# Performance work log

Hardware: AMD Instinct MI355X
Metric: run time of the kernel (lower is better)

The kernel has to match this reference:

```python
import jax, jax.numpy as jnp
import numpy as np
import math

H = 12  # num_heads
LOGIT_SCALE_MAX = math.log(1.0 / 0.01)  # ~4.60517


def setup_inputs() -> dict:
    key = jax.random.key(0)
    ks = jax.random.split(key, 4)
    L, N, C = 1024, 8, 768
    scale = (C // H) ** -0.5
    return {
        "x": jax.random.normal(ks[0], (L, N, C), jnp.float32),
        "in_proj_weight": jax.random.normal(ks[1], (3 * C, C), jnp.float32) * scale,
        "in_proj_bias": jnp.zeros((3 * C,), jnp.float32),
        "logit_scale": jnp.full((H, 1, 1), jnp.log(10.0), jnp.float32),
        "head_scale": jnp.ones((H, 1, 1), jnp.float32),
        "out_w": jax.random.normal(ks[2], (C, C), jnp.float32) * scale,
        "out_b": jnp.zeros((C,), jnp.float32),
    }


def _normalize(t, eps=1e-12):
    # torch F.normalize: x / max(||x||, eps)
    n = jnp.linalg.norm(t, axis=-1, keepdims=True)
    return t / jnp.maximum(n, eps)


def reference(x, in_proj_weight, in_proj_bias, logit_scale, head_scale, out_w, out_b):
    L, N, C = x.shape
    D = C // H
    qkv = x @ in_proj_weight.T + in_proj_bias  # (L, N, 3C)
    q, k, v = jnp.split(qkv, 3, axis=-1)

    def to_heads(t):  # (L, N, C) -> (N, H, L, D); matches view(L, N*H, D).transpose(0,1)
        return t.reshape(L, N, H, D).transpose(1, 2, 0, 3)

    q, k, v = to_heads(q), to_heads(k), to_heads(v)
    # scaled-cosine attention: cosine sim * clamped-exp learnable logit scale
    attn = jnp.einsum('nhld,nhmd->nhlm', _normalize(q), _normalize(k))  # (N,H,L,L)
    ls = jnp.exp(jnp.minimum(logit_scale, LOGIT_SCALE_MAX))  # (H,1,1)
    attn = attn * ls[None]
    attn = jax.nn.softmax(attn, axis=-1)
    o = jnp.einsum('nhlm,nhmd->nhld', attn, v)  # (N,H,L,D)
    o = o * head_scale[None]  # per-head scale
    o = o.transpose(2, 0, 1, 3).reshape(L, N, C)  # back to (L, N, C)
    return o @ out_w.T + out_b
```

## Files before the change

kernel.cpp:

```cpp
#include <hip/hip_runtime.h>
#include <stdint.h>
#include <math.h>

typedef unsigned short u16;
typedef _Float16 f16;
typedef __attribute__((ext_vector_type(4))) float f32x4;
typedef __attribute__((ext_vector_type(8))) f16 h8;
typedef __attribute__((ext_vector_type(4))) f16 h4;
typedef __attribute__((ext_vector_type(2))) f16 h2;
typedef __attribute__((ext_vector_type(2))) __fp16 fp16x2;
typedef __attribute__((ext_vector_type(2))) unsigned int u32x2;
typedef __attribute__((ext_vector_type(4))) unsigned int u32x4;
typedef __attribute__((ext_vector_type(4))) unsigned short u16x4;
typedef __attribute__((ext_vector_type(8))) unsigned short u16x8;

typedef const __attribute__((address_space(1))) u16 gas_u16;
typedef __attribute__((address_space(3))) u16 las_u16;

#define MFMA32(a,b,c) __builtin_amdgcn_mfma_f32_16x16x32_f16((a),(b),(c),0,0,0)
#define MFMA16(a,b,c) __builtin_amdgcn_mfma_f32_16x16x16f16((a),(b),(c),0,0,0)

__device__ __forceinline__ float h2f(u16 h){ f16 x; __builtin_memcpy(&x,&h,2); return (float)x; }
__device__ __forceinline__ u16 f2h(float f){ f16 x = (f16)f; u16 u; __builtin_memcpy(&u,&x,2); return u; }

__device__ __forceinline__ float fast_exp2(float x){
#if __has_builtin(__builtin_amdgcn_exp2f)
  return __builtin_amdgcn_exp2f(x);
#else
  return exp2f(x);
#endif
}

__device__ __forceinline__ h2 pkrtz(float a, float b){
  fp16x2 t = __builtin_amdgcn_cvt_pkrtz(a, b);
  h2 r; __builtin_memcpy(&r, &t, 4);
  return r;
}

#define NA4 1572864
#define NB4 442368
#define NC4 147456
__global__ __launch_bounds__(256) void cvt3_kernel(
    const float* __restrict__ a, u16* __restrict__ da,
    const float* __restrict__ b, u16* __restrict__ db,
    const float* __restrict__ c, u16* __restrict__ dc)
{
  int i = blockIdx.x*256 + threadIdx.x;
  const float* s; u16* d; int off;
  if (i < NA4)            { s = a; d = da; off = i; }
  else if (i < NA4+NB4)   { s = b; d = db; off = i - NA4; }
  else if (i < NA4+NB4+NC4){ s = c; d = dc; off = i - NA4 - NB4; }
  else return;
  f32x4 v = ((const f32x4*)s)[off];
  u16x4 o;
  o[0]=f2h(v[0]); o[1]=f2h(v[1]); o[2]=f2h(v[2]); o[3]=f2h(v[3]);
  ((u16x4*)d)[off] = o;
}

__global__ __launch_bounds__(256) void gemm_kernel(
    const u16* __restrict__ A, const u16* __restrict__ B, const float* __restrict__ bias,
    int mode, u16* __restrict__ qh, u16* __restrict__ kh, u16* __restrict__ vtp,
    float* __restrict__ outp, const float* __restrict__ lsb)
{
  __shared__ u16 lA[2][128*64];
  __shared__ u16 lB[2][128*64];
  const int tid = threadIdx.x;
  const int lane = tid & 63;
  const int w = tid >> 6, wr = w >> 1, wc = w & 1;
  const int lo = lane & 15, hi = lane >> 4;

  const int bx = blockIdx.x, by = blockIdx.y;

  f32x4 zero = {0.f,0.f,0.f,0.f};
  f32x4 acc[4][4];
#pragma unroll
  for (int a=0;a<4;a++)
#pragma unroll
    for (int b=0;b<4;b++) acc[a][b] = zero;
  const u16* Ag = A + (size_t)bx*128*768;
  const u16* Bg = B + (size_t)by*128*768;
  const int srow = tid >> 3;
  const int scol = (((tid & 7) ^ (srow & 7)) * 8);

#define STAGE(buf, kt) do { \
    _Pragma("unroll") \
    for (int j=0;j<4;j++) { \
      __builtin_amdgcn_global_load_lds((gas_u16*)(Ag + (size_t)(j*32+srow)*768 + (kt) + scol), (las_u16*)(&lA[buf][j*2048 + tid*8]), 16, 0, 0); \
      __builtin_amdgcn_global_load_lds((gas_u16*)(Bg + (size_t)(j*32+srow)*768 + (kt) + scol), (las_u16*)(&lB[buf][j*2048 + tid*8]), 16, 0, 0); \
    } \
  } while(0)

  STAGE(0, 0);
#pragma unroll
  for (int t = 0; t < 12; ++t) {
    const int cur = t & 1;
    if (t < 11) {
      STAGE(cur^1, (t+1)*64);
      asm volatile("s_waitcnt vmcnt(8)" ::: "memory");
    } else {
      asm volatile("s_waitcnt vmcnt(0)" ::: "memory");
    }
    __builtin_amdgcn_sched_barrier(0);
    __builtin_amdgcn_s_barrier();
#pragma unroll
    for (int kk=0;kk<2;kk++) {
      h8 af[4], bfr[4];
#pragma unroll
      for (int mf=0; mf<4; mf++) {
        int r = wr*64 + mf*16 + lo;
        af[mf]  = *(const h8*)(&lA[cur][r*64 + (((hi + 4*kk) ^ (lo & 7)) * 8)]);
      }
#pragma unroll
      for (int nf=0; nf<4; nf++) {
        int r = wc*64 + nf*16 + lo;
        bfr[nf] = *(const h8*)(&lB[cur][r*64 + (((hi + 4*kk) ^ (lo & 7)) * 8)]);
      }
#pragma unroll
      for (int mf=0; mf<4; mf++)
#pragma unroll
        for (int nf=0; nf<4; nf++)
          acc[mf][nf] = MFMA32(af[mf], bfr[nf], acc[mf][nf]);
    }
    asm volatile("s_waitcnt lgkmcnt(0)" ::: "memory");
    __builtin_amdgcn_sched_barrier(0);
    __builtin_amdgcn_s_barrier();
  }
#undef STAGE

  const int r0 = bx*128 + wr*64;
  const int j0 = by*128 + wc*64;
  if (mode == 0) {
    const int p = (j0 >= 1536) ? 2 : ((j0 >= 768) ? 1 : 0);
    float bi[4];
#pragma unroll
    for (int nf=0;nf<4;nf++) bi[nf] = bias[j0 + nf*16 + lo];
    if (p == 2) {
      u16* Tt = (wc == 0) ? (u16*)lA : (u16*)lB;
      const int cbase = wr*16;
#pragma unroll
      for (int mf=0; mf<4; mf++)
#pragma unroll
        for (int nf=0; nf<4; nf++) {
          int d = nf*16 + lo;
          int c = cbase + mf*4 + hi;
          u16x4 pk;
#pragma unroll
          for (int i=0;i<4;i++) pk[i] = f2h(acc[mf][nf][i] + bi[nf]);
          *(u16x4*)(Tt + d*128 + ((c ^ ((d & 7) << 2)) << 2)) = pk;
        }
      __syncthreads();
      const int hh0 = 2*by - 24;
#pragma unroll
      for (int kq=0; kq<8; kq++) {
        int idx = tid + kq*256;
        int nn  = idx & 7;
        int d   = (idx >> 3) & 63;
        int lh  = (idx >> 9) & 1;
        int wcc = idx >> 10;
        const u16* Ts = (wcc == 0) ? (const u16*)lA : (const u16*)lB;
        u16x8 v8;
#pragma unroll
        for (int ll=0; ll<8; ll++) {
          int rl = (lh*8 + ll)*8 + nn;
          int c  = rl >> 2;
          v8[ll] = Ts[d*128 + ((c ^ ((d & 7) << 2)) << 2) + (rl & 3)];
        }
        size_t off = (((size_t)nn*12 + hh0 + wcc)*64 + d)*1024 + (size_t)bx*16 + lh*8;
        *(u16x8*)(vtp + off) = v8;
      }
    } else {
      const int c0 = j0 - p*768;
      const int hh = c0 >> 6;
      u16* dst = (p==0) ? qh : kh;
      float qsc = 1.0f;
      if (p == 0) qsc = __expf(fminf(lsb[hh], 4.6051701859880913680f)) * 1.4426950408889634f;
#pragma unroll
      for (int mf=0; mf<4; mf++)
#pragma unroll
        for (int i=0;i<4;i++) {
          int r = r0 + mf*16 + 4*hi + i;
          int n = r & 7, l = r >> 3;
          float v[4]; float ss = 0.f;
#pragma unroll
          for (int nf=0;nf<4;nf++){ v[nf] = acc[mf][nf][i] + bi[nf]; ss += v[nf]*v[nf]; }
          ss += __shfl_xor(ss, 1);
          ss += __shfl_xor(ss, 2);
          ss += __shfl_xor(ss, 4);
          ss += __shfl_xor(ss, 8);
          float sc = qsc / fmaxf(sqrtf(ss), 1e-12f);
          size_t base = (((size_t)n*12 + hh)*1024 + l)*64;
#pragma unroll
          for (int nf=0;nf<4;nf++)
            dst[base + nf*16 + lo] = f2h(v[nf]*sc);
        }
    }
  } else {
#pragma unroll
    for (int nf=0; nf<4; nf++) {
      int j = j0 + nf*16 + lo;
      float bi = bias[j];
#pragma unroll
      for (int mf=0; mf<4; mf++)
#pragma unroll
        for (int i=0;i<4;i++) {
          int r = r0 + mf*16 + 4*hi + i;
          outp[(size_t)r*768 + j] = acc[mf][nf][i] + bi;
        }
    }
  }
}

__global__ __launch_bounds__(256, 6) void flash_kernel(
    const u16* __restrict__ qh, const u16* __restrict__ kh, const u16* __restrict__ vt,
    u16* __restrict__ obuf, const float* __restrict__ hsv, const float* __restrict__ lsp)
{
  __shared__ u16 lK[64*64];
  __shared__ u16 lVT[64*64];
  const int lin = blockIdx.y*16 + blockIdx.x;
  const int xcd = lin & 7, g = lin >> 3;
  const int nh = xcd + 8*(g >> 4);
  const int qt = g & 15;
  const int h = nh % 12, n = nh / 12;
  const u16* Qp = qh + (size_t)nh*65536;
  const u16* Kp = kh + (size_t)nh*65536;
  const u16* Vp = vt + (size_t)nh*65536;
  const int tid = threadIdx.x, lane = tid & 63, w = tid >> 6;
  const int lo = lane & 15, hi = lane >> 4;
  const int e = lo & 7;

  h8 qa0, qa1;
  {
    const u16* qrow = Qp + (size_t)(qt*64 + w*16 + lo)*64 + hi*8;
    qa0 = *(const h8*)qrow;
    qa1 = *(const h8*)(qrow + 32);
  }
  const f32x4 zero = {0.f,0.f,0.f,0.f};
  f32x4 oA[4] = {zero,zero,zero,zero};
  f32x4 lA4 = zero;
  const h4 ones = {(f16)1.f,(f16)1.f,(f16)1.f,(f16)1.f};

  float OFF;
  {
    float b = __expf(fminf(lsp[h], 4.6051701859880913680f)) * 1.4426950408889634f;
    OFF = fmaxf(b - 15.5f, 0.f);
  }

  const int sr = tid >> 2;
  const int c4 = tid & 3;
  const int sx1 = sr & 7;
  const int sx2 = (sr & 7) << 1;

  u32x4 ka, kb, va, vb;
  ka = *(const u32x4*)(Kp + (size_t)sr*64 + c4*16);
  kb = *(const u32x4*)(Kp + (size_t)sr*64 + c4*16 + 8);
  va = *(const u32x4*)(Vp + (size_t)sr*1024 + c4*16);
  vb = *(const u32x4*)(Vp + (size_t)sr*1024 + c4*16 + 8);

  for (int t = 0; t < 16; ++t) {
    {
      u16* kr = lK + sr*64;
      *(u32x4*)(kr + (((2*c4)   ^ sx1) << 3)) = ka;
      *(u32x4*)(kr + (((2*c4+1) ^ sx1) << 3)) = kb;
      u16* vr = lVT + sr*64;
      *(u32x2*)(vr + (((( 0|c4) ^ sx2) << 2))) = (u32x2){va[0], va[1]};
      *(u32x2*)(vr + (((( 4|c4) ^ sx2) << 2))) = (u32x2){va[2], va[3]};
      *(u32x2*)(vr + (((( 8|c4) ^ sx2) << 2))) = (u32x2){vb[0], vb[1]};
      *(u32x2*)(vr + ((((12|c4) ^ sx2) << 2))) = (u32x2){vb[2], vb[3]};
    }
    asm volatile("s_waitcnt lgkmcnt(0)" ::: "memory");
    __builtin_amdgcn_sched_barrier(0);
    __builtin_amdgcn_s_barrier();
    if (t < 15) {
      ka = *(const u32x4*)(Kp + (size_t)(t+1)*4096 + (size_t)sr*64 + c4*16);
      kb = *(const u32x4*)(Kp + (size_t)(t+1)*4096 + (size_t)sr*64 + c4*16 + 8);
      va = *(const u32x4*)(Vp + (size_t)sr*1024 + (t+1)*64 + c4*16);
      vb = *(const u32x4*)(Vp + (size_t)sr*1024 + (t+1)*64 + c4*16 + 8);
    }
    f32x4 sa[4];
#pragma unroll
    for (int kf=0; kf<4; kf++) {
      const u16* krow = lK + (kf*16 + lo)*64;
      h8 k0 = *(const h8*)(krow + (((hi  ) ^ e) << 3));
      h8 k1 = *(const h8*)(krow + (((hi+4) ^ e) << 3));
      sa[kf] = MFMA32(k1, qa1, MFMA32(k0, qa0, zero));
    }
    if (OFF != 0.f) {
#pragma unroll
      for (int kf=0;kf<4;kf++)
#pragma unroll
        for (int i=0;i<4;i++) sa[kf][i] -= OFF;
    }
    h4 pa[4];
#pragma unroll
    for (int kf=0;kf<4;kf++) {
      h2 a01 = pkrtz(fast_exp2(sa[kf][0]), fast_exp2(sa[kf][1]));
      h2 a23 = pkrtz(fast_exp2(sa[kf][2]), fast_exp2(sa[kf][3]));
      pa[kf] = __builtin_shufflevector(a01, a23, 0, 1, 2, 3);
    }
#pragma unroll
    for (int kf=0;kf<4;kf++) lA4 = MFMA16(ones, pa[kf], lA4);
#pragma unroll
    for (int db=0; db<4; db++) {
      const u16* vrow = lVT + (db*16 + lo)*64;
      h8 v01 = *(const h8*)(vrow + ((((2*hi  ) ^ e) << 3)));
      h8 v23 = *(const h8*)(vrow + ((((2*hi+1) ^ e) << 3)));
      oA[db] = MFMA16(__builtin_shufflevector(v01, v01, 0,1,2,3), pa[0], oA[db]);
      oA[db] = MFMA16(__builtin_shufflevector(v01, v01, 4,5,6,7), pa[1], oA[db]);
      oA[db] = MFMA16(__builtin_shufflevector(v23, v23, 0,1,2,3), pa[2], oA[db]);
      oA[db] = MFMA16(__builtin_shufflevector(v23, v23, 4,5,6,7), pa[3], oA[db]);
    }
    asm volatile("s_waitcnt lgkmcnt(0)" ::: "memory");
    __builtin_amdgcn_sched_barrier(0);
    __builtin_amdgcn_s_barrier();
  }
  float inv = hsv[h] / lA4[0];
  int l = qt*64 + w*16 + lo;
  u16* dst = obuf + ((size_t)l*8 + n)*768 + h*64;
#pragma unroll
  for (int db=0; db<4; db++) {
    u16x4 pk;
#pragma unroll
    for (int i=0;i<4;i++) pk[i] = f2h(oA[db][i] * inv);
    *(u16x4*)(dst + db*16 + hi*4) = pk;
  }
}

extern "C" void kernel_launch(void* const* d_in, const int* in_sizes, int n_in,
                              void* d_out, int out_size, void* d_ws, size_t ws_size,
                              hipStream_t stream)
{
  (void)in_sizes; (void)n_in; (void)out_size; (void)ws_size;
  const float* x  = (const float*)d_in[0];
  const float* w1 = (const float*)d_in[1];
  const float* b1 = (const float*)d_in[2];
  const float* ls = (const float*)d_in[3];
  const float* hs = (const float*)d_in[4];
  const float* w2 = (const float*)d_in[5];
  const float* b2 = (const float*)d_in[6];
  float* out = (float*)d_out;

  u16* x_bf  = (u16*)d_ws;
  u16* w1_bf = x_bf  + 6291456;
  u16* w2_bf = w1_bf + 1769472;
  u16* qh    = w2_bf + 589824;
  u16* kh    = qh    + 6291456;
  u16* vt    = kh    + 6291456;
  u16* ob    = x_bf;

  cvt3_kernel<<<8448, 256, 0, stream>>>(x, x_bf, w1, w1_bf, w2, w2_bf);
  gemm_kernel<<<dim3(64,18), 256, 0, stream>>>(x_bf, w1_bf, b1, 0, qh, kh, vt, nullptr, ls);
  flash_kernel<<<dim3(16,96), 256, 0, stream>>>(qh, kh, vt, ob, hs, ls);
  gemm_kernel<<<dim3(64,6), 256, 0, stream>>>(ob, w2_bf, b2, 1, nullptr, nullptr, nullptr, out, ls);
}
```

Baseline: 123.7 us.

## Double query rows per flash block to reuse K/V tiles across two fragments

Each flash-attention block now handles 128 query rows instead of 64, with every wave computing two 16-row fragments that share the same K and V loads from LDS. The grid is halved and launch bounds drop to 3 blocks per SM to make room for the extra accumulator registers. The aim is to halve the global-to-LDS traffic per query and cut LDS reads per MFMA. The cost is lower occupancy, fewer blocks (768) in the grid, and higher register pressure.

```diff
diff --git a/kernel.cpp b/kernel.cpp
--- a/kernel.cpp
+++ b/kernel.cpp
@@ -210,16 +210,16 @@
   }
 }
 
-__global__ __launch_bounds__(256, 6) void flash_kernel(
+__global__ __launch_bounds__(256, 3) void flash_kernel(
     const u16* __restrict__ qh, const u16* __restrict__ kh, const u16* __restrict__ vt,
     u16* __restrict__ obuf, const float* __restrict__ hsv, const float* __restrict__ lsp)
 {
   __shared__ u16 lK[64*64];
   __shared__ u16 lVT[64*64];
-  const int lin = blockIdx.y*16 + blockIdx.x;
+  const int lin = blockIdx.y*8 + blockIdx.x;
   const int xcd = lin & 7, g = lin >> 3;
-  const int nh = xcd + 8*(g >> 4);
-  const int qt = g & 15;
+  const int nh = xcd + 8*(g >> 3);
+  const int qt = g & 7;
   const int h = nh % 12, n = nh / 12;
   const u16* Qp = qh + (size_t)nh*65536;
   const u16* Kp = kh + (size_t)nh*65536;
@@ -228,15 +228,16 @@
   const int lo = lane & 15, hi = lane >> 4;
   const int e = lo & 7;
 
-  h8 qa0, qa1;
+  h8 qa0, qa1, qb0, qb1;
   {
-    const u16* qrow = Qp + (size_t)(qt*64 + w*16 + lo)*64 + hi*8;
-    qa0 = *(const h8*)qrow;
-    qa1 = *(const h8*)(qrow + 32);
+    const u16* qrow = Qp + (size_t)(qt*128 + w*32 + lo)*64 + hi*8;
+    qa0 = *(const h8*)qrow;          qa1 = *(const h8*)(qrow + 32);
+    qb0 = *(const h8*)(qrow + 1024); qb1 = *(const h8*)(qrow + 1024 + 32);
   }
   const f32x4 zero = {0.f,0.f,0.f,0.f};
   f32x4 oA[4] = {zero,zero,zero,zero};
-  f32x4 lA4 = zero;
+  f32x4 oB[4] = {zero,zero,zero,zero};
+  f32x4 lA4 = zero, lB4 = zero;
   const h4 ones = {(f16)1.f,(f16)1.f,(f16)1.f,(f16)1.f};
 
   float OFF;
@@ -276,52 +277,71 @@
       va = *(const u32x4*)(Vp + (size_t)sr*1024 + (t+1)*64 + c4*16);
       vb = *(const u32x4*)(Vp + (size_t)sr*1024 + (t+1)*64 + c4*16 + 8);
     }
-    f32x4 sa[4];
+    f32x4 sa[4], sb[4];
 #pragma unroll
     for (int kf=0; kf<4; kf++) {
       const u16* krow = lK + (kf*16 + lo)*64;
       h8 k0 = *(const h8*)(krow + (((hi  ) ^ e) << 3));
       h8 k1 = *(const h8*)(krow + (((hi+4) ^ e) << 3));
       sa[kf] = MFMA32(k1, qa1, MFMA32(k0, qa0, zero));
+      sb[kf] = MFMA32(k1, qb1, MFMA32(k0, qb0, zero));
     }
     if (OFF != 0.f) {
 #pragma unroll
       for (int kf=0;kf<4;kf++)
 #pragma unroll
-        for (int i=0;i<4;i++) sa[kf][i] -= OFF;
-    }
-    h4 pa[4];
+        for (int i=0;i<4;i++) { sa[kf][i] -= OFF; sb[kf][i] -= OFF; }
+    }
+    h4 pa[4], pb[4];
 #pragma unroll
     for (int kf=0;kf<4;kf++) {
       h2 a01 = pkrtz(fast_exp2(sa[kf][0]), fast_exp2(sa[kf][1]));
       h2 a23 = pkrtz(fast_exp2(sa[kf][2]), fast_exp2(sa[kf][3]));
       pa[kf] = __builtin_shufflevector(a01, a23, 0, 1, 2, 3);
-    }
-#pragma unroll
-    for (int kf=0;kf<4;kf++) lA4 = MFMA16(ones, pa[kf], lA4);
+      h2 b01 = pkrtz(fast_exp2(sb[kf][0]), fast_exp2(sb[kf][1]));
+      h2 b23 = pkrtz(fast_exp2(sb[kf][2]), fast_exp2(sb[kf][3]));
+      pb[kf] = __builtin_shufflevector(b01, b23, 0, 1, 2, 3);
+    }
+#pragma unroll
+    for (int kf=0;kf<4;kf++) {
+      lA4 = MFMA16(ones, pa[kf], lA4);
+      lB4 = MFMA16(ones, pb[kf], lB4);
+    }
 #pragma unroll
     for (int db=0; db<4; db++) {
       const u16* vrow = lVT + (db*16 + lo)*64;
       h8 v01 = *(const h8*)(vrow + ((((2*hi  ) ^ e) << 3)));
       h8 v23 = *(const h8*)(vrow + ((((2*hi+1) ^ e) << 3)));
-      oA[db] = MFMA16(__builtin_shufflevector(v01, v01, 0,1,2,3), pa[0], oA[db]);
-      oA[db] = MFMA16(__builtin_shufflevector(v01, v01, 4,5,6,7), pa[1], oA[db]);
-      oA[db] = MFMA16(__builtin_shufflevector(v23, v23, 0,1,2,3), pa[2], oA[db]);
-      oA[db] = MFMA16(__builtin_shufflevector(v23, v23, 4,5,6,7), pa[3], oA[db]);
+      h4 f0 = __builtin_shufflevector(v01, v01, 0,1,2,3);
+      h4 f1 = __builtin_shufflevector(v01, v01, 4,5,6,7);
+      h4 f2 = __builtin_shufflevector(v23, v23, 0,1,2,3);
+      h4 f3 = __builtin_shufflevector(v23, v23, 4,5,6,7);
+      oA[db] = MFMA16(f0, pa[0], oA[db]);
+      oB[db] = MFMA16(f0, pb[0], oB[db]);
+      oA[db] = MFMA16(f1, pa[1], oA[db]);
+      oB[db] = MFMA16(f1, pb[1], oB[db]);
+      oA[db] = MFMA16(f2, pa[2], oA[db]);
+      oB[db] = MFMA16(f2, pb[2], oB[db]);
+      oA[db] = MFMA16(f3, pa[3], oA[db]);
+      oB[db] = MFMA16(f3, pb[3], oB[db]);
     }
     asm volatile("s_waitcnt lgkmcnt(0)" ::: "memory");
     __builtin_amdgcn_sched_barrier(0);
     __builtin_amdgcn_s_barrier();
   }
-  float inv = hsv[h] / lA4[0];
-  int l = qt*64 + w*16 + lo;
-  u16* dst = obuf + ((size_t)l*8 + n)*768 + h*64;
+  float hsc = hsv[h];
+  float invA = hsc / lA4[0];
+  float invB = hsc / lB4[0];
+  int l0 = qt*128 + w*32 + lo;
+  u16* dA = obuf + ((size_t)l0*8 + n)*768 + h*64;
+  u16* dB = obuf + ((size_t)(l0+16)*8 + n)*768 + h*64;
 #pragma unroll
   for (int db=0; db<4; db++) {
-    u16x4 pk;
-#pragma unroll
-    for (int i=0;i<4;i++) pk[i] = f2h(oA[db][i] * inv);
-    *(u16x4*)(dst + db*16 + hi*4) = pk;
+    u16x4 pk0, pk1;
+#pragma unroll
+    for (int i=0;i<4;i++) { pk0[i] = f2h(oA[db][i]*invA); pk1[i] = f2h(oB[db][i]*invB); }
+    *(u16x4*)(dA + db*16 + hi*4) = pk0;
+    *(u16x4*)(dB + db*16 + hi*4) = pk1;
   }
 }
 
@@ -349,6 +369,6 @@
 
   cvt3_kernel<<<8448, 256, 0, stream>>>(x, x_bf, w1, w1_bf, w2, w2_bf);
   gemm_kernel<<<dim3(64,18), 256, 0, stream>>>(x_bf, w1_bf, b1, 0, qh, kh, vt, nullptr, ls);
-  flash_kernel<<<dim3(16,96), 256, 0, stream>>>(qh, kh, vt, ob, hs, ls);
+  flash_kernel<<<dim3(8,96), 256, 0, stream>>>(qh, kh, vt, ob, hs, ls);
   gemm_kernel<<<dim3(64,6), 256, 0, stream>>>(ob, w2_bf, b2, 1, nullptr, nullptr, nullptr, out, ls);
 }
```

Measured after the change: 118.3 us. 4.4% less time.
